# Kernel optimization log

Measured on AMD Instinct MI355X. Metric: run time of the kernel, lower is better.

The kernel has to match this reference:

```python
import jax, jax.numpy as jnp
import numpy as np

D_MODEL = 1024
N_HEAD = 16
D_K = D_MODEL // N_HEAD
D_FF = 4096
B, S = 4, 2048


def setup_inputs() -> dict:
    key = jax.random.key(0)
    ks = jax.random.split(key, 16)
    sd = 1.0 / np.sqrt(D_MODEL)
    sf = 1.0 / np.sqrt(D_FF)
    inp = {
        'x': jax.random.normal(ks[0], (B, S, D_MODEL), dtype=jnp.float32),
        'mask': jnp.ones((B, 1, S), dtype=jnp.int32),
        # attention projections (stored as [in, out] so y = x @ W + b)
        'wq': jax.random.normal(ks[1], (D_MODEL, D_MODEL), dtype=jnp.float32) * sd,
        'bq': jnp.zeros((D_MODEL,), dtype=jnp.float32),
        'wk': jax.random.normal(ks[2], (D_MODEL, D_MODEL), dtype=jnp.float32) * sd,
        'bk': jnp.zeros((D_MODEL,), dtype=jnp.float32),
        'wv': jax.random.normal(ks[3], (D_MODEL, D_MODEL), dtype=jnp.float32) * sd,
        'bv': jnp.zeros((D_MODEL,), dtype=jnp.float32),
        'wo': jax.random.normal(ks[4], (D_MODEL, D_MODEL), dtype=jnp.float32) * sd,
        'bo': jnp.zeros((D_MODEL,), dtype=jnp.float32),
        # feedforward
        'w1': jax.random.normal(ks[5], (D_MODEL, D_FF), dtype=jnp.float32) * sd,
        'b1': jnp.zeros((D_FF,), dtype=jnp.float32),
        'w2': jax.random.normal(ks[6], (D_FF, D_MODEL), dtype=jnp.float32) * sf,
        'b2': jnp.zeros((D_MODEL,), dtype=jnp.float32),
        # Tensor1DNorm params
        'alpha1': jnp.ones((D_MODEL,), dtype=jnp.float32),
        'bias1': jnp.zeros((D_MODEL,), dtype=jnp.float32),
        'alpha2': jnp.ones((D_MODEL,), dtype=jnp.float32),
        'bias2': jnp.zeros((D_MODEL,), dtype=jnp.float32),
    }
    return inp


def _norm(x, alpha, bias, eps=1e-6):
    # Tensor1DNorm: uses unbiased std (torch default, ddof=1), eps added to std
    mean = jnp.mean(x, axis=-1, keepdims=True)
    std = jnp.std(x, axis=-1, keepdims=True, ddof=1)
    return alpha * (x - mean) / (std + eps) + bias


def _encoder_layer(x, mask, wq, bq, wk, bk, wv, bv, wo, bo, w1, b1, w2, b2,
                   alpha1, bias1, alpha2, bias2):
    # --- self-attention sublayer (pre-norm) ---
    x2 = _norm(x, alpha1, bias1)
    Bn = x2.shape[0]
    q = (x2 @ wq + bq).reshape(Bn, -1, N_HEAD, D_K).transpose(0, 2, 1, 3)  # [B,H,S,dk]
    k = (x2 @ wk + bk).reshape(Bn, -1, N_HEAD, D_K).transpose(0, 2, 1, 3)
    v = (x2 @ wv + bv).reshape(Bn, -1, N_HEAD, D_K).transpose(0, 2, 1, 3)
    scores = jnp.einsum('bhqd,bhkd->bhqk', q, k) / jnp.sqrt(jnp.float32(D_K))
    # mask unsqueezed at dim 1 in torch: [B,1,S] -> [B,1,1,S]
    scores = jnp.where(mask[:, None, :, :] == 0, jnp.float32(-1e9), scores)
    p = jax.nn.softmax(scores, axis=-1)
    attn_out = jnp.einsum('bhqk,bhkd->bhqd', p, v)
    attn_out = attn_out.transpose(0, 2, 1, 3).reshape(Bn, -1, N_HEAD * D_K)
    x = x + (attn_out @ wo + bo)
    # --- feedforward sublayer (pre-norm) ---
    x2 = _norm(x, alpha2, bias2)
    ff = jax.nn.relu(x2 @ w1 + b1) @ w2 + b2
    return x + ff


def reference(x, mask, wq, bq, wk, bk, wv, bv, wo, bo, w1, b1, w2, b2,
              alpha1, bias1, alpha2, bias2):
    return _encoder_layer(x, mask, wq, bq, wk, bk, wv, bv, wo, bo,
                          w1, b1, w2, b2, alpha1, bias1, alpha2, bias2)
```

## Files before the change

kernel.cpp:

```cpp
#include <hip/hip_runtime.h>

#define D_MODEL 1024
#define D_FF    4096
#define N_HEADS 16
#define DK      64
#define BATCH   4
#define SEQ     2048
#define M_TOT   (BATCH*SEQ)

typedef unsigned short ushort_t;
typedef __attribute__((ext_vector_type(8))) short  short8;
typedef __attribute__((ext_vector_type(4))) float  floatx4;

__device__ __forceinline__ float bf2f(ushort_t s) {
    return __uint_as_float(((unsigned int)s) << 16);
}
__device__ __forceinline__ ushort_t f2bf(float f) {
    unsigned int u = __float_as_uint(f);
    u += 0x7fff + ((u >> 16) & 1);
    return (ushort_t)(u >> 16);
}
__device__ __forceinline__ void gll16(const void* g, void* l) {
    __builtin_amdgcn_global_load_lds(
        (const __attribute__((address_space(1))) void*)g,
        (__attribute__((address_space(3))) void*)l,
        16, 0, 0);
}

#if __has_builtin(__builtin_amdgcn_exp2f)
#define EXP2(x) __builtin_amdgcn_exp2f(x)
#else
#define EXP2(x) __expf((x) * 0.69314718055994531f)
#endif
#define L2E 1.4426950408889634f

__global__ void detect_dtype(const ushort_t* __restrict__ x, int* __restrict__ flag)
{
    const int t = threadIdx.x;
    int cnt = 0;
    for (int i = t; i < 512; i += 64) {
        ushort_t e = x[2 * i] & 0x7F80;
        cnt += (e >= 0x3800 && e <= 0x4380) ? 1 : 0;
    }
    for (int off = 32; off > 0; off >>= 1) cnt += __shfl_down(cnt, off, 64);
    if (t == 0) { flag[0] = (cnt >= 256) ? 1 : 0; flag[1] = 0; }
}

__global__ void cvt_params(
    const void* bq, const void* bk, const void* bv, const void* bo,
    const void* b1, const void* b2, const void* a1, const void* be1,
    const void* a2, const void* be2, float* __restrict__ dst,
    const int* __restrict__ flag)
{
    const int e = blockIdx.x * 256 + threadIdx.x;
    const int seg = e >> 10;
    const void* srcs[13] = {bq, bk, bv, bo, b1, b1, b1, b1, b2, a1, be1, a2, be2};
    const int   base[13] = {0, 1024, 2048, 3072, 4096, 4096, 4096, 4096,
                            8192, 9216, 10240, 11264, 12288};
    const void* s = srcs[seg];
    const int off = e - base[seg];
    const float scale = (seg == 0) ? 0.125f : 1.f;
    float v = (*flag) ? bf2f(((const ushort_t*)s)[off]) : ((const float*)s)[off];
    dst[e] = v * scale;
}

__device__ __forceinline__ void transpose_body(
    const void* __restrict__ in, ushort_t* __restrict__ out, int K, int N,
    float scale, int fl, ushort_t* tile, int n0, int k0)
{
    const int t = threadIdx.x, sr = t >> 2, sc = (t & 3) * 16;
    const long g = (long)(k0 + sr) * N + n0 + sc;
    ushort_t cv[16];
    if (fl) {
        const ushort_t* p = (const ushort_t*)in;
        #pragma unroll
        for (int j = 0; j < 16; j++) cv[j] = f2bf(bf2f(p[g + j]) * scale);
    } else {
        const float* p = (const float*)in;
        #pragma unroll
        for (int j = 0; j < 16; j += 4) {
            float4 fv = *(const float4*)&p[g + j];
            cv[j] = f2bf(fv.x * scale); cv[j+1] = f2bf(fv.y * scale);
            cv[j+2] = f2bf(fv.z * scale); cv[j+3] = f2bf(fv.w * scale);
        }
    }
    #pragma unroll
    for (int j = 0; j < 16; j++) tile[sr * 72 + sc + j] = cv[j];
    __syncthreads();
    __attribute__((aligned(16))) ushort_t tmp[16];
    #pragma unroll
    for (int j = 0; j < 16; j++) tmp[j] = tile[(sc + j) * 72 + sr];
    const long go = (long)(n0 + sr) * K + k0 + sc;
    *(int4*)&out[go]     = *(const int4*)&tmp[0];
    *(int4*)&out[go + 8] = *(const int4*)&tmp[8];
}

__global__ __launch_bounds__(256) void transpose_to_bf16(
    const void* __restrict__ in, ushort_t* __restrict__ out, int K, int N,
    float scale, const int* __restrict__ flag)
{
    __shared__ ushort_t tile[64 * 72];
    transpose_body(in, out, K, N, scale, *flag, tile,
                   blockIdx.x * 64, blockIdx.y * 64);
}

__global__ __launch_bounds__(256) void transpose_qkvo(
    const void* __restrict__ wq, const void* __restrict__ wk,
    const void* __restrict__ wv, const void* __restrict__ wo,
    ushort_t* __restrict__ out, const int* __restrict__ flag)
{
    __shared__ ushort_t tile[64 * 72];
    const int z = blockIdx.z;
    const void* in = (z == 0) ? wq : (z == 1) ? wk : (z == 2) ? wv : wo;
    transpose_body(in, out + (long)z * 1024 * 1024, 1024, 1024,
                   (z == 0) ? 0.125f : 1.f, *flag, tile,
                   blockIdx.x * 64, blockIdx.y * 64);
}

__global__ __launch_bounds__(256) void ln_kernel(
    const void* __restrict__ xraw, const float* __restrict__ alpha,
    const float* __restrict__ beta, ushort_t* __restrict__ out,
    const int* __restrict__ flag)
{
    __shared__ float red[8];
    __shared__ float stats[2];
    const int row = blockIdx.x, t = threadIdx.x;
    const long idx = (long)row * D_MODEL + t * 4;
    float v0, v1, v2, v3;
    if (*flag) {
        ushort4 u = *(const ushort4*)&((const ushort_t*)xraw)[idx];
        v0 = bf2f(u.x); v1 = bf2f(u.y); v2 = bf2f(u.z); v3 = bf2f(u.w);
    } else {
        float4 fv = *(const float4*)&((const float*)xraw)[idx];
        v0 = fv.x; v1 = fv.y; v2 = fv.z; v3 = fv.w;
    }
    float s  = v0 + v1 + v2 + v3;
    float s2 = v0 * v0 + v1 * v1 + v2 * v2 + v3 * v3;
    for (int off = 32; off > 0; off >>= 1) {
        s  += __shfl_down(s,  off, 64);
        s2 += __shfl_down(s2, off, 64);
    }
    const int w = t >> 6, lane = t & 63;
    if (lane == 0) { red[w] = s; red[4 + w] = s2; }
    __syncthreads();
    if (t == 0) {
        float S  = red[0] + red[1] + red[2] + red[3];
        float S2 = red[4] + red[5] + red[6] + red[7];
        float mean = S / D_MODEL;
        float var  = fmaxf((S2 - mean * S) / (D_MODEL - 1), 0.f);
        stats[0] = mean;
        stats[1] = 1.f / (sqrtf(var) + 1e-6f);
    }
    __syncthreads();
    const float mean = stats[0], inv = stats[1];
    float vv[4] = {v0, v1, v2, v3};
    ushort4 o;
    ushort_t* op = (ushort_t*)&o;
    #pragma unroll
    for (int j = 0; j < 4; j++)
        op[j] = f2bf(alpha[t * 4 + j] * (vv[j] - mean) * inv + beta[t * 4 + j]);
    *(ushort4*)&out[idx] = o;
}

#define GEMM_PROLOG()                                                         \
    __shared__ ushort_t As[128 * 64];                                         \
    __shared__ ushort_t Bs[128 * 64];                                         \
    const int m0 = blockIdx.x * 128, n0 = blockIdx.y * 128;                   \
    const int t = threadIdx.x;                                                \
    const int w = t >> 6, lane = t & 63, quad = lane >> 4, l15 = lane & 15;   \
    const int wm = (w >> 1) * 64, wn = (w & 1) * 64;                          \
    const int srow = lane >> 3;                         \
    const int scol = 8 * ((lane & 7) ^ (srow & 7));     \
    const int rswz = (l15 & 7) * 8;                        \
    floatx4 acc[4][4] = {};

#define GEMM_KLOOP(Abase, LDA, Bbase, LDB, KLEN)                              \
    {                                                                         \
    const ushort_t* gA = (Abase) + (long)(m0 + w * 32 + srow) * (LDA) + scol; \
    const ushort_t* gB = (Bbase) + (long)(n0 + w * 32 + srow) * (LDB) + scol; \
    for (int k0 = 0; k0 < (KLEN); k0 += 64) {                                 \
        _Pragma("unroll")                                                     \
        for (int c = 0; c < 4; c++) {                                         \
            gll16(gA + k0 + (long)(c * 8) * (LDA), &As[(w * 32 + c * 8) * 64]);\
            gll16(gB + k0 + (long)(c * 8) * (LDB), &Bs[(w * 32 + c * 8) * 64]);\
        }                                                                     \
        __syncthreads();                                                      \
        _Pragma("unroll")                                                     \
        for (int kk = 0; kk < 2; kk++) {                                      \
            short8 af[4], bf[4];                                              \
            _Pragma("unroll")                                                 \
            for (int i = 0; i < 4; i++)                                       \
                af[i] = *(const short8*)&As[(wm + i * 16 + l15) * 64 +        \
                        ((kk * 32 + quad * 8) ^ rswz)];                       \
            _Pragma("unroll")                                                 \
            for (int j = 0; j < 4; j++)                                       \
                bf[j] = *(const short8*)&Bs[(wn + j * 16 + l15) * 64 +        \
                        ((kk * 32 + quad * 8) ^ rswz)];                       \
            _Pragma("unroll")                                                 \
            for (int i = 0; i < 4; i++) {                                     \
                _Pragma("unroll")                                             \
                for (int j = 0; j < 4; j++)                                   \
                    acc[i][j] = __builtin_amdgcn_mfma_f32_16x16x32_bf16(      \
                        af[i], bf[j], acc[i][j], 0, 0, 0);                    \
            }                                                                 \
        }                                                                     \
        __syncthreads();                                                      \
    }                                                                         \
    }

__global__ __launch_bounds__(256) void gemm_qkv(
    const ushort_t* __restrict__ A, const ushort_t* __restrict__ BT,
    const float* __restrict__ bias, ushort_t* __restrict__ qb,
    ushort_t* __restrict__ kb, ushort_t* __restrict__ vtb, int M, int K)
{
    GEMM_PROLOG();
    GEMM_KLOOP(A, K, BT, K, K);
    const int nbase = n0 + wn;
    const int seg = nbase >> 10;
    #pragma unroll
    for (int j = 0; j < 4; j++) {
        const int ng = nbase + j * 16 + l15;
        const float bv = bias[ng];
        const int nl = ng & 1023;
        #pragma unroll
        for (int i = 0; i < 4; i++) {
            const int mb_ = m0 + wm + i * 16 + quad * 4;
            if (seg == 2) {
                ushort4 pv;
                #pragma unroll
                for (int r = 0; r < 4; r++)
                    ((ushort_t*)&pv)[r] = f2bf(acc[i][j][r] + bv);
                const long idx = ((long)(mb_ >> 11) * 1024 + nl) * 2048 + (mb_ & 2047);
                *(ushort4*)&vtb[idx] = pv;
            } else {
                ushort_t* dst = seg ? kb : qb;
                #pragma unroll
                for (int r = 0; r < 4; r++)
                    dst[(long)(mb_ + r) * 1024 + nl] = f2bf(acc[i][j][r] + bv);
            }
        }
    }
}

__global__ __launch_bounds__(256) void gemm_bias_res_trunk(
    const ushort_t* __restrict__ A, const ushort_t* __restrict__ BT,
    const float* __restrict__ bias, const void* __restrict__ res,
    float* __restrict__ C, int M, int N, int K, const int* __restrict__ flag)
{
    GEMM_PROLOG();
    const int fl = *flag;
    GEMM_KLOOP(A, K, BT, K, K);
    #pragma unroll
    for (int j = 0; j < 4; j++) {
        const int n = n0 + wn + j * 16 + l15;
        const float bv = bias[n];
        #pragma unroll
        for (int i = 0; i < 4; i++) {
            const int mbase = m0 + wm + i * 16 + quad * 4;
            #pragma unroll
            for (int r = 0; r < 4; r++) {
                const long idx = (long)(mbase + r) * N + n;
                const float rv = fl ? bf2f(((const ushort_t*)res)[idx])
                                    : ((const float*)res)[idx];
                C[idx] = acc[i][j][r] + bv + rv;
            }
        }
    }
}

__global__ __launch_bounds__(256) void gemm_relu_slice(
    const ushort_t* __restrict__ A, const ushort_t* __restrict__ BT,
    const float* __restrict__ bias, ushort_t* __restrict__ C,
    int M, int Nc, int K, int noff)
{
    GEMM_PROLOG();
    const ushort_t* BTo = BT + (long)noff * K;
    GEMM_KLOOP(A, K, BTo, K, K);
    #pragma unroll
    for (int j = 0; j < 4; j++) {
        const int n = n0 + wn + j * 16 + l15;
        const float bv = bias[noff + n];
        #pragma unroll
        for (int i = 0; i < 4; i++) {
            const int mbase = m0 + wm + i * 16 + quad * 4;
            #pragma unroll
            for (int r = 0; r < 4; r++)
                C[(long)(mbase + r) * Nc + n] = f2bf(fmaxf(acc[i][j][r] + bv, 0.f));
        }
    }
}

__global__ __launch_bounds__(256) void gemm_acc_slice(
    const ushort_t* __restrict__ A, const ushort_t* __restrict__ BT,
    const float* __restrict__ bias, float* __restrict__ C,
    int M, int N, int Kc, int koff, int Kfull, int pass0)
{
    GEMM_PROLOG();
    const ushort_t* BTo = BT + koff;
    GEMM_KLOOP(A, Kc, BTo, Kfull, Kc);
    #pragma unroll
    for (int j = 0; j < 4; j++) {
        const int n = n0 + wn + j * 16 + l15;
        const float bv = pass0 ? bias[n] : 0.f;
        #pragma unroll
        for (int i = 0; i < 4; i++) {
            const int mbase = m0 + wm + i * 16 + quad * 4;
            #pragma unroll
            for (int r = 0; r < 4; r++) {
                const long idx = (long)(mbase + r) * N + n;
                C[idx] = C[idx] + bv + acc[i][j][r];
            }
        }
    }
}

__global__ __launch_bounds__(256) void gemm_acc_final(
    const ushort_t* __restrict__ A, const ushort_t* __restrict__ BT,
    const float* __restrict__ Cin, void* __restrict__ out,
    int M, int N, int Kc, int koff, int Kfull, const int* __restrict__ flag)
{
    GEMM_PROLOG();
    const int fl = *flag;
    const ushort_t* BTo = BT + koff;
    GEMM_KLOOP(A, Kc, BTo, Kfull, Kc);
    #pragma unroll
    for (int j = 0; j < 4; j++) {
        const int n = n0 + wn + j * 16 + l15;
        #pragma unroll
        for (int i = 0; i < 4; i++) {
            const int mbase = m0 + wm + i * 16 + quad * 4;
            #pragma unroll
            for (int r = 0; r < 4; r++) {
                const long idx = (long)(mbase + r) * N + n;
                const float v = Cin[idx] + acc[i][j][r];
                if (fl) ((ushort_t*)out)[idx] = f2bf(v);
                else    ((float*)out)[idx] = v;
            }
        }
    }
}

__global__ __launch_bounds__(256) void finalize_out(
    const float* __restrict__ trunk, void* __restrict__ out,
    const int* __restrict__ flag)
{
    const long i = ((long)blockIdx.x * 256 + threadIdx.x) * 4;
    float4 tv = *(const float4*)&trunk[i];
    if (*flag) {
        ushort4 o = { f2bf(tv.x), f2bf(tv.y), f2bf(tv.z), f2bf(tv.w) };
        *(ushort4*)&((ushort_t*)out)[i] = o;
    } else {
        *(float4*)&((float*)out)[i] = tv;
    }
}

__global__ __launch_bounds__(256) void attn_kernel(
    const ushort_t* __restrict__ q, const ushort_t* __restrict__ k,
    const ushort_t* __restrict__ vt, const int* __restrict__ mask,
    ushort_t* __restrict__ out)
{
    __shared__ ushort_t Ks[64 * 72];
    __shared__ ushort_t Vs[64 * 72];
    __shared__ ushort_t Ps[128 * 72];
    __shared__ float MbL[64];
    const int qt = blockIdx.x, bh = blockIdx.y;
    const int b = bh >> 4, h = bh & 15;
    const int t = threadIdx.x, w = t >> 6, lane = t & 63;
    const int quad = lane >> 4, l15 = lane & 15;
    const int sr = t >> 2, sc = (t & 3) * 16;
    const int q0 = qt * 128;
    const long rowbase = (long)b * SEQ * D_MODEL + (long)h * DK;
    const long vtbase  = ((long)(b * 16 + h) * DK) * SEQ;

    {
        const int qr = t >> 1, qc = (t & 1) * 32;
        const long g = rowbase + (long)(q0 + qr) * D_MODEL + qc;
        *(int4*)&Ps[qr * 72 + qc]      = *(const int4*)&q[g];
        *(int4*)&Ps[qr * 72 + qc + 8]  = *(const int4*)&q[g + 8];
        *(int4*)&Ps[qr * 72 + qc + 16] = *(const int4*)&q[g + 16];
        *(int4*)&Ps[qr * 72 + qc + 24] = *(const int4*)&q[g + 24];
    }
    short8 bq[2][2];
    #pragma unroll
    for (int qg = 0; qg < 2; qg++)
        #pragma unroll
        for (int ks = 0; ks < 2; ks++)
            bq[qg][ks] = *(const short8*)&Ps[(w * 32 + qg * 16 + l15) * 72 + ks * 32 + quad * 8];

    short8 bones;
    #pragma unroll
    for (int i = 0; i < 8; i++) bones[i] = (short)0x3F80;

    floatx4 o[2][4] = {};
    floatx4 l4[2] = {};

    int4 kra, krb, vra, vrb;
    int  mreg = 0;
    {
        const long gk = rowbase + (long)sr * D_MODEL + sc;
        kra = *(const int4*)&k[gk]; krb = *(const int4*)&k[gk + 8];
        const long gv = vtbase + (long)sr * SEQ + sc;
        vra = *(const int4*)&vt[gv]; vrb = *(const int4*)&vt[gv + 8];
        if (t < 64) mreg = mask[b * SEQ + t];
    }

    for (int kt = 0; kt < SEQ / 64; kt++) {
        __syncthreads();
        *(int4*)&Ks[sr * 72 + sc]     = kra;
        *(int4*)&Ks[sr * 72 + sc + 8] = krb;
        *(int4*)&Vs[sr * 72 + sc]     = vra;
        *(int4*)&Vs[sr * 72 + sc + 8] = vrb;
        if (t < 64) MbL[t] = (mreg == 0) ? -1.0e9f : -44.0f;
        __syncthreads();
        if (kt + 1 < SEQ / 64) {
            const long gk = rowbase + (long)((kt + 1) * 64 + sr) * D_MODEL + sc;
            kra = *(const int4*)&k[gk]; krb = *(const int4*)&k[gk + 8];
            const long gv = vtbase + (long)sr * SEQ + (kt + 1) * 64 + sc;
            vra = *(const int4*)&vt[gv]; vrb = *(const int4*)&vt[gv + 8];
            if (t < 64) mreg = mask[b * SEQ + (kt + 1) * 64 + t];
        }

        floatx4 s[4][2] = {};
        __builtin_amdgcn_s_setprio(1);
        #pragma unroll
        for (int nt = 0; nt < 4; nt++) {
            short8 ak0 = *(const short8*)&Ks[(nt * 16 + l15) * 72 + quad * 8];
            s[nt][0] = __builtin_amdgcn_mfma_f32_16x16x32_bf16(ak0, bq[0][0], s[nt][0], 0, 0, 0);
            s[nt][1] = __builtin_amdgcn_mfma_f32_16x16x32_bf16(ak0, bq[1][0], s[nt][1], 0, 0, 0);
            short8 ak1 = *(const short8*)&Ks[(nt * 16 + l15) * 72 + 32 + quad * 8];
            s[nt][0] = __builtin_amdgcn_mfma_f32_16x16x32_bf16(ak1, bq[0][1], s[nt][0], 0, 0, 0);
            s[nt][1] = __builtin_amdgcn_mfma_f32_16x16x32_bf16(ak1, bq[1][1], s[nt][1], 0, 0, 0);
        }
        __builtin_amdgcn_s_setprio(0);

        #pragma unroll
        for (int qg = 0; qg < 2; qg++) {
            #pragma unroll
            for (int nt = 0; nt < 4; nt++) {
                float4 mb4 = *(const float4*)&MbL[nt * 16 + quad * 4];
                float p[4];
                #pragma unroll
                for (int r = 0; r < 4; r++)
                    p[r] = EXP2(fmaf(s[nt][qg][r], L2E, ((const float*)&mb4)[r]));
                uint2 pk;
                pk.x = __builtin_amdgcn_perm(__float_as_uint(p[1]), __float_as_uint(p[0]), 0x07060302u);
                pk.y = __builtin_amdgcn_perm(__float_as_uint(p[3]), __float_as_uint(p[2]), 0x07060302u);
                *(uint2*)&Ps[(w * 32 + qg * 16 + l15) * 72 + nt * 16 + quad * 4] = pk;
            }
        }

        __builtin_amdgcn_s_setprio(1);
        #pragma unroll
        for (int ks = 0; ks < 2; ks++) {
            short8 ap0 = *(const short8*)&Ps[(w * 32 + l15) * 72 + ks * 32 + quad * 8];
            short8 ap1 = *(const short8*)&Ps[(w * 32 + 16 + l15) * 72 + ks * 32 + quad * 8];
            #pragma unroll
            for (int j = 0; j < 4; j++) {
                short8 bv = *(const short8*)&Vs[(j * 16 + l15) * 72 + ks * 32 + quad * 8];
                o[0][j] = __builtin_amdgcn_mfma_f32_16x16x32_bf16(ap0, bv, o[0][j], 0, 0, 0);
                o[1][j] = __builtin_amdgcn_mfma_f32_16x16x32_bf16(ap1, bv, o[1][j], 0, 0, 0);
            }
            l4[0] = __builtin_amdgcn_mfma_f32_16x16x32_bf16(ap0, bones, l4[0], 0, 0, 0);
            l4[1] = __builtin_amdgcn_mfma_f32_16x16x32_bf16(ap1, bones, l4[1], 0, 0, 0);
        }
        __builtin_amdgcn_s_setprio(0);
    }
    #pragma unroll
    for (int qg = 0; qg < 2; qg++) {
        float inv[4];
        #pragma unroll
        for (int r = 0; r < 4; r++) inv[r] = 1.f / l4[qg][r];
        #pragma unroll
        for (int j = 0; j < 4; j++) {
            const int d = j * 16 + l15;
            #pragma unroll
            for (int r = 0; r < 4; r++) {
                const int row = q0 + w * 32 + qg * 16 + quad * 4 + r;
                out[rowbase + (long)row * D_MODEL + d] = f2bf(o[qg][j][r] * inv[r]);
            }
        }
    }
}

extern "C" void kernel_launch(void* const* d_in, const int* in_sizes, int n_in,
                              void* d_out, int out_size, void* d_ws, size_t ws_size,
                              hipStream_t stream)
{
    const void* x      = d_in[0];
    const int*  mask   = (const int*)d_in[1];
    const void* wq     = d_in[2];
    const void* bq     = d_in[3];
    const void* wk     = d_in[4];
    const void* bk     = d_in[5];
    const void* wv     = d_in[6];
    const void* bv     = d_in[7];
    const void* wo     = d_in[8];
    const void* bo     = d_in[9];
    const void* w1     = d_in[10];
    const void* b1     = d_in[11];
    const void* w2     = d_in[12];
    const void* b2     = d_in[13];
    const void* alpha1 = d_in[14];
    const void* bias1  = d_in[15];
    const void* alpha2 = d_in[16];
    const void* bias2  = d_in[17];

    char* ws = (char*)d_ws;
    const size_t MB = 1024 * 1024;
    const size_t KB = 1024;
    ushort_t* wqkvT = (ushort_t*)(ws + 0 * MB);
    ushort_t* woT   = (ushort_t*)(ws + 6 * MB);
    ushort_t* w1T   = (ushort_t*)(ws + 8 * MB);
    ushort_t* w2T   = (ushort_t*)(ws + 16 * MB);
    float* pb    = (float*)(ws + 24 * MB);
    float* bqkvf = pb + 0;
    float* bof   = pb + 3072;
    float* b1f   = pb + 4096;
    float* b2f   = pb + 8192;
    float* a1f   = pb + 9216;
    float* be1f  = pb + 10240;
    float* a2f   = pb + 11264;
    float* be2f  = pb + 12288;
    int*   flag  = (int*)(ws + 24 * MB + 8 * 16 * KB);
    int*   flagz = flag + 1;
    ushort_t* lnbuf = (ushort_t*)(ws + 25 * MB);
    ushort_t* qb    = (ushort_t*)(ws + 41 * MB);
    ushort_t* kb    = (ushort_t*)(ws + 57 * MB);
    ushort_t* vtb   = (ushort_t*)(ws + 73 * MB);
    ushort_t* attnb = lnbuf;

    const bool bigws   = (ws_size >= 121ull * MB);
    const bool outf32  = (out_size == (int)(sizeof(float) * M_TOT * D_MODEL));

    dim3 blk(256);
    detect_dtype<<<1, 64, 0, stream>>>((const ushort_t*)x, flag);

    cvt_params<<<52, blk, 0, stream>>>(bq, bk, bv, bo, b1, b2,
                                       alpha1, bias1, alpha2, bias2, pb, flag);

    transpose_qkvo<<<dim3(16, 16, 4), blk, 0, stream>>>(wq, wk, wv, wo, wqkvT, flag);
    transpose_to_bf16<<<dim3(64, 16), blk, 0, stream>>>(w1, w1T, D_MODEL, D_FF, 1.f, flag);
    transpose_to_bf16<<<dim3(16, 64), blk, 0, stream>>>(w2, w2T, D_FF, D_MODEL, 1.f, flag);

    ln_kernel<<<M_TOT, blk, 0, stream>>>(x, a1f, be1f, lnbuf, flag);

    gemm_qkv<<<dim3(64, 24), blk, 0, stream>>>(lnbuf, wqkvT, bqkvf, qb, kb, vtb,
                                               M_TOT, D_MODEL);

    attn_kernel<<<dim3(SEQ / 128, BATCH * N_HEADS), blk, 0, stream>>>(qb, kb, vtb, mask, attnb);

    if (bigws) {
        float*    trunk   = (float*)kb;
        ushort_t* ln2buf  = qb;
        ushort_t* halfbuf = (ushort_t*)(ws + 89 * MB);
        gemm_bias_res_trunk<<<dim3(64, 8), blk, 0, stream>>>(attnb, woT, bof, x, trunk,
                                                             M_TOT, D_MODEL, D_MODEL, flag);
        ln_kernel<<<M_TOT, blk, 0, stream>>>(trunk, a2f, be2f, ln2buf, flagz);
        gemm_relu_slice<<<dim3(64, 16), blk, 0, stream>>>(ln2buf, w1T, b1f, halfbuf,
                                                          M_TOT, 2048, D_MODEL, 0);
        gemm_acc_slice<<<dim3(64, 8), blk, 0, stream>>>(halfbuf, w2T, b2f, trunk,
                                                        M_TOT, D_MODEL, 2048, 0, D_FF, 1);
        gemm_relu_slice<<<dim3(64, 16), blk, 0, stream>>>(ln2buf, w1T, b1f, halfbuf,
                                                          M_TOT, 2048, D_MODEL, 2048);
        gemm_acc_final<<<dim3(64, 8), blk, 0, stream>>>(halfbuf, w2T, trunk, d_out,
                                                        M_TOT, D_MODEL, 2048, 2048, D_FF, flag);
    } else if (outf32) {
        float*    trunk   = (float*)kb;
        ushort_t* ln2buf  = qb;
        ushort_t* halfbuf = (ushort_t*)d_out;
        gemm_bias_res_trunk<<<dim3(64, 8), blk, 0, stream>>>(attnb, woT, bof, x, trunk,
                                                             M_TOT, D_MODEL, D_MODEL, flag);
        ln_kernel<<<M_TOT, blk, 0, stream>>>(trunk, a2f, be2f, ln2buf, flagz);
        gemm_relu_slice<<<dim3(64, 16), blk, 0, stream>>>(ln2buf, w1T, b1f, halfbuf,
                                                          M_TOT, 2048, D_MODEL, 0);
        gemm_acc_slice<<<dim3(64, 8), blk, 0, stream>>>(halfbuf, w2T, b2f, trunk,
                                                        M_TOT, D_MODEL, 2048, 0, D_FF, 1);
        gemm_relu_slice<<<dim3(64, 16), blk, 0, stream>>>(ln2buf, w1T, b1f, halfbuf,
                                                          M_TOT, 2048, D_MODEL, 2048);
        gemm_acc_slice<<<dim3(64, 8), blk, 0, stream>>>(halfbuf, w2T, b2f, trunk,
                                                        M_TOT, D_MODEL, 2048, 2048, D_FF, 0);
        finalize_out<<<M_TOT * D_MODEL / 1024, blk, 0, stream>>>(trunk, d_out, flag);
    } else {
        float*    trunk   = (float*)qb;
        ushort_t* ln2buf  = vtb;
        ushort_t* halfbuf = lnbuf;
        gemm_bias_res_trunk<<<dim3(64, 8), blk, 0, stream>>>(attnb, woT, bof, x, trunk,
                                                             M_TOT, D_MODEL, D_MODEL, flag);
        ln_kernel<<<M_TOT, blk, 0, stream>>>(trunk, a2f, be2f, ln2buf, flagz);
        for (int qtr = 0; qtr < 4; qtr++) {
            const int off = qtr * 1024;
            gemm_relu_slice<<<dim3(64, 8), blk, 0, stream>>>(ln2buf, w1T, b1f, halfbuf,
                                                             M_TOT, 1024, D_MODEL, off);
            gemm_acc_slice<<<dim3(64, 8), blk, 0, stream>>>(halfbuf, w2T, b2f, trunk,
                                                            M_TOT, D_MODEL, 1024, off,
                                                            D_FF, qtr == 0 ? 1 : 0);
        }
        finalize_out<<<M_TOT * D_MODEL / 1024, blk, 0, stream>>>(trunk, d_out, flag);
    }
}
```

Before: 580.3 us.

## Use 256x256-tile 8-wave GEMM with async double buffering for QKV and FFN1

After: 586.7 us. No clear change (+1.1%).

```diff
diff --git a/kernel.cpp b/kernel.cpp
--- a/kernel.cpp
+++ b/kernel.cpp
@@ -208,14 +208,80 @@
     }                                                                         \
     }
 
-__global__ __launch_bounds__(256) void gemm_qkv(
+#define G8_PROLOG()                                                           \
+    __shared__ ushort_t As8[2][256 * 64];                                     \
+    __shared__ ushort_t Bs8[2][256 * 64];                                     \
+    const int m0 = blockIdx.x * 256, n0 = blockIdx.y * 256;                   \
+    const int tid = threadIdx.x;                                              \
+    const int wid = tid >> 6, lane = tid & 63;                                \
+    const int quad = lane >> 4, l15 = lane & 15;                              \
+    const int wr = wid >> 2, wc = wid & 3;                                    \
+    const int srow = lane >> 3;                                               \
+    const int scol = 8 * ((lane & 7) ^ (srow & 7));                           \
+    const int rswz = (l15 & 7) * 8;                                           \
+    floatx4 acc[8][4] = {};
+
+#define G8_STAGE(buf, Abase, LDA, Bbase, LDB, ktile)                          \
+    {                                                                         \
+    const ushort_t* gA_ = (Abase) + (long)(m0 + wid * 32 + srow) * (LDA)      \
+                          + (ktile) * 64 + scol;                              \
+    const ushort_t* gB_ = (Bbase) + (long)(n0 + wid * 32 + srow) * (LDB)      \
+                          + (ktile) * 64 + scol;                              \
+    _Pragma("unroll")                                                         \
+    for (int c = 0; c < 4; c++) {                                             \
+        gll16(gA_ + (long)(c * 8) * (LDA), &As8[buf][(wid * 32 + c * 8) * 64]);\
+        gll16(gB_ + (long)(c * 8) * (LDB), &Bs8[buf][(wid * 32 + c * 8) * 64]);\
+    }                                                                         \
+    }
+
+#define G8_KLOOP(Abase, LDA, Bbase, LDB, KLEN)                                \
+    {                                                                         \
+    const int T_ = (KLEN) / 64;                                               \
+    G8_STAGE(0, Abase, LDA, Bbase, LDB, 0);                                   \
+    G8_STAGE(1, Abase, LDA, Bbase, LDB, 1);                                   \
+    for (int t_ = 0; t_ < T_; t_++) {                                         \
+        const int cur = t_ & 1;                                               \
+        if (t_ + 1 < T_) { asm volatile("s_waitcnt vmcnt(8)" ::: "memory"); } \
+        else             { asm volatile("s_waitcnt vmcnt(0)" ::: "memory"); } \
+        __builtin_amdgcn_s_barrier();                                         \
+        _Pragma("unroll")                                                     \
+        for (int kk = 0; kk < 2; kk++) {                                      \
+            const int kc = (kk * 32 + quad * 8) ^ rswz;                       \
+            short8 bf[4];                                                     \
+            _Pragma("unroll")                                                 \
+            for (int j = 0; j < 4; j++)                                       \
+                bf[j] = *(const short8*)&Bs8[cur][(wc * 64 + j * 16 + l15) * 64 + kc]; \
+            _Pragma("unroll")                                                 \
+            for (int ih = 0; ih < 2; ih++) {                                  \
+                short8 af[4];                                                 \
+                _Pragma("unroll")                                             \
+                for (int i2 = 0; i2 < 4; i2++)                                \
+                    af[i2] = *(const short8*)&As8[cur][(wr * 128 +            \
+                             (ih * 4 + i2) * 16 + l15) * 64 + kc];            \
+                __builtin_amdgcn_s_setprio(1);                                \
+                _Pragma("unroll")                                             \
+                for (int i2 = 0; i2 < 4; i2++) {                              \
+                    _Pragma("unroll")                                         \
+                    for (int j = 0; j < 4; j++)                               \
+                        acc[ih * 4 + i2][j] = __builtin_amdgcn_mfma_f32_16x16x32_bf16( \
+                            af[i2], bf[j], acc[ih * 4 + i2][j], 0, 0, 0);     \
+                }                                                             \
+                __builtin_amdgcn_s_setprio(0);                                \
+            }                                                                 \
+        }                                                                     \
+        __builtin_amdgcn_s_barrier();                                         \
+        if (t_ + 2 < T_) { G8_STAGE(cur, Abase, LDA, Bbase, LDB, t_ + 2); }   \
+    }                                                                         \
+    }
+
+__global__ __launch_bounds__(512, 2) void gemm_qkv8(
     const ushort_t* __restrict__ A, const ushort_t* __restrict__ BT,
     const float* __restrict__ bias, ushort_t* __restrict__ qb,
     ushort_t* __restrict__ kb, ushort_t* __restrict__ vtb, int M, int K)
 {
-    GEMM_PROLOG();
-    GEMM_KLOOP(A, K, BT, K, K);
-    const int nbase = n0 + wn;
+    G8_PROLOG();
+    G8_KLOOP(A, K, BT, K, K);
+    const int nbase = n0 + wc * 64;
     const int seg = nbase >> 10;
     #pragma unroll
     for (int j = 0; j < 4; j++) {
@@ -223,8 +289,8 @@
         const float bv = bias[ng];
         const int nl = ng & 1023;
         #pragma unroll
-        for (int i = 0; i < 4; i++) {
-            const int mb_ = m0 + wm + i * 16 + quad * 4;
+        for (int i = 0; i < 8; i++) {
+            const int mb_ = m0 + wr * 128 + i * 16 + quad * 4;
             if (seg == 2) {
                 ushort4 pv;
                 #pragma unroll
@@ -238,6 +304,28 @@
                 for (int r = 0; r < 4; r++)
                     dst[(long)(mb_ + r) * 1024 + nl] = f2bf(acc[i][j][r] + bv);
             }
+        }
+    }
+}
+
+__global__ __launch_bounds__(512, 2) void gemm_relu8(
+    const ushort_t* __restrict__ A, const ushort_t* __restrict__ BT,
+    const float* __restrict__ bias, ushort_t* __restrict__ C,
+    int M, int Nc, int K, int noff)
+{
+    G8_PROLOG();
+    const ushort_t* BTo = BT + (long)noff * K;
+    G8_KLOOP(A, K, BTo, K, K);
+    #pragma unroll
+    for (int j = 0; j < 4; j++) {
+        const int n = n0 + wc * 64 + j * 16 + l15;
+        const float bv = bias[noff + n];
+        #pragma unroll
+        for (int i = 0; i < 8; i++) {
+            const int mb_ = m0 + wr * 128 + i * 16 + quad * 4;
+            #pragma unroll
+            for (int r = 0; r < 4; r++)
+                C[(long)(mb_ + r) * Nc + n] = f2bf(fmaxf(acc[i][j][r] + bv, 0.f));
         }
     }
 }
@@ -533,6 +621,7 @@
     const bool outf32  = (out_size == (int)(sizeof(float) * M_TOT * D_MODEL));
 
     dim3 blk(256);
+    dim3 blk8(512);
     detect_dtype<<<1, 64, 0, stream>>>((const ushort_t*)x, flag);
 
     cvt_params<<<52, blk, 0, stream>>>(bq, bk, bv, bo, b1, b2,
@@ -544,8 +633,8 @@
 
     ln_kernel<<<M_TOT, blk, 0, stream>>>(x, a1f, be1f, lnbuf, flag);
 
-    gemm_qkv<<<dim3(64, 24), blk, 0, stream>>>(lnbuf, wqkvT, bqkvf, qb, kb, vtb,
-                                               M_TOT, D_MODEL);
+    gemm_qkv8<<<dim3(32, 12), blk8, 0, stream>>>(lnbuf, wqkvT, bqkvf, qb, kb, vtb,
+                                                 M_TOT, D_MODEL);
 
     attn_kernel<<<dim3(SEQ / 128, BATCH * N_HEADS), blk, 0, stream>>>(qb, kb, vtb, mask, attnb);
 
@@ -556,12 +645,12 @@
         gemm_bias_res_trunk<<<dim3(64, 8), blk, 0, stream>>>(attnb, woT, bof, x, trunk,
                                                              M_TOT, D_MODEL, D_MODEL, flag);
         ln_kernel<<<M_TOT, blk, 0, stream>>>(trunk, a2f, be2f, ln2buf, flagz);
-        gemm_relu_slice<<<dim3(64, 16), blk, 0, stream>>>(ln2buf, w1T, b1f, halfbuf,
-                                                          M_TOT, 2048, D_MODEL, 0);
+        gemm_relu8<<<dim3(32, 8), blk8, 0, stream>>>(ln2buf, w1T, b1f, halfbuf,
+                                                     M_TOT, 2048, D_MODEL, 0);
         gemm_acc_slice<<<dim3(64, 8), blk, 0, stream>>>(halfbuf, w2T, b2f, trunk,
                                                         M_TOT, D_MODEL, 2048, 0, D_FF, 1);
-        gemm_relu_slice<<<dim3(64, 16), blk, 0, stream>>>(ln2buf, w1T, b1f, halfbuf,
-                                                          M_TOT, 2048, D_MODEL, 2048);
+        gemm_relu8<<<dim3(32, 8), blk8, 0, stream>>>(ln2buf, w1T, b1f, halfbuf,
+                                                     M_TOT, 2048, D_MODEL, 2048);
         gemm_acc_final<<<dim3(64, 8), blk, 0, stream>>>(halfbuf, w2T, trunk, d_out,
                                                         M_TOT, D_MODEL, 2048, 2048, D_FF, flag);
     } else if (outf32) {
@@ -571,12 +660,12 @@
         gemm_bias_res_trunk<<<dim3(64, 8), blk, 0, stream>>>(attnb, woT, bof, x, trunk,
                                                              M_TOT, D_MODEL, D_MODEL, flag);
         ln_kernel<<<M_TOT, blk, 0, stream>>>(trunk, a2f, be2f, ln2buf, flagz);
-        gemm_relu_slice<<<dim3(64, 16), blk, 0, stream>>>(ln2buf, w1T, b1f, halfbuf,
-                                                          M_TOT, 2048, D_MODEL, 0);
+        gemm_relu8<<<dim3(32, 8), blk8, 0, stream>>>(ln2buf, w1T, b1f, halfbuf,
+                                                     M_TOT, 2048, D_MODEL, 0);
         gemm_acc_slice<<<dim3(64, 8), blk, 0, stream>>>(halfbuf, w2T, b2f, trunk,
                                                         M_TOT, D_MODEL, 2048, 0, D_FF, 1);
-        gemm_relu_slice<<<dim3(64, 16), blk, 0, stream>>>(ln2buf, w1T, b1f, halfbuf,
-                                                          M_TOT, 2048, D_MODEL, 2048);
+        gemm_relu8<<<dim3(32, 8), blk8, 0, stream>>>(ln2buf, w1T, b1f, halfbuf,
+                                                     M_TOT, 2048, D_MODEL, 2048);
         gemm_acc_slice<<<dim3(64, 8), blk, 0, stream>>>(halfbuf, w2T, b2f, trunk,
                                                         M_TOT, D_MODEL, 2048, 2048, D_FF, 0);
         finalize_out<<<M_TOT * D_MODEL / 1024, blk, 0, stream>>>(trunk, d_out, flag);
```
